# Kernel tuning notes

Hardware: AMD Instinct MI355X
Metric: run time of the kernel (lower is better)

## Reference

```python
import jax, jax.numpy as jnp
import numpy as np

N_E, N_U, N_D = 512, 256, 256
N_A = 16
N_FB = 4
N_SV = 256
N_PV = 64
D_IN0 = 3 * (4 * N_A) + 2 * 4   # 200, fb_block output at layer 0
D_IN = 3 * N_SV + 2 * N_PV      # 896, fb_block output thereafter


def _fb_block(s_v, p_v):
    # s_v: (n_e, d_s); p_v: (n_e, n_e, d_p)
    n_e = N_U + N_D
    su_m = jnp.tile(s_v[:N_U].mean(0)[None, :], (n_e, 1))
    sd_m = jnp.tile(s_v[N_U:].mean(0)[None, :], (n_e, 1))
    pu_m = p_v[:N_U].mean(0)   # (n_e, d_p)
    pd_m = p_v[N_U:].mean(0)
    return jnp.concatenate([su_m, sd_m, pu_m, pd_m, s_v], axis=-1)


def setup_inputs() -> dict:
    key = jax.random.key(0)
    ks = jax.random.split(key, 16)

    def lin(k, fin, fout):
        k1, k2 = jax.random.split(k)
        lim = 1.0 / np.sqrt(fin)
        W = jax.random.uniform(k1, (fin, fout), minval=-lim, maxval=lim, dtype=jnp.float32)
        b = jax.random.uniform(k2, (fout,), minval=-lim, maxval=lim, dtype=jnp.float32)
        return W, b

    V0_W, V0_b = lin(ks[0], D_IN0, N_SV)
    W0_W, W0_b = lin(ks[1], 4, N_PV)
    VrW, Vrb, WrW, Wrb = [], [], [], []
    for i in range(N_FB - 1):
        w, b = lin(ks[2 + i], D_IN, N_SV); VrW.append(w); Vrb.append(b)
        w, b = lin(ks[6 + i], N_PV, N_PV); WrW.append(w); Wrb.append(b)
    Vr_W, Vr_b = jnp.stack(VrW), jnp.stack(Vrb)
    Wr_W, Wr_b = jnp.stack(WrW), jnp.stack(Wrb)
    Vhu_W, Vhu_b = lin(ks[10], D_IN, N_SV)
    Vhd_W, Vhd_b = lin(ks[11], D_IN, N_SV)
    wu_W, wu_b = lin(ks[12], N_SV, N_U)
    wd_W, wd_b = lin(ks[13], N_SV, N_D)
    r = jax.random.normal(ks[14], (N_E, 3), dtype=jnp.float32)
    a = jax.random.normal(ks[15], (N_A, 3), dtype=jnp.float32) * 2.0
    return dict(r=r, a=a, V0_W=V0_W, V0_b=V0_b, Vr_W=Vr_W, Vr_b=Vr_b,
                W0_W=W0_W, W0_b=W0_b, Wr_W=Wr_W, Wr_b=Wr_b,
                Vhu_W=Vhu_W, Vhu_b=Vhu_b, Vhd_W=Vhd_W, Vhd_b=Vhd_b,
                wu_W=wu_W, wu_b=wu_b, wd_W=wd_W, wd_b=wd_b)


def reference(r, a, V0_W, V0_b, Vr_W, Vr_b, W0_W, W0_b, Wr_W, Wr_b,
              Vhu_W, Vhu_b, Vhd_W, Vhd_b, wu_W, wu_b, wd_W, wd_b):
    n_e = N_E
    eye = jnp.eye(n_e, dtype=r.dtype)[:, :, None]
    ra = r[:, None, :] - a[None, :, :]                       # (n_e, n_a, 3)
    ra_len = jnp.linalg.norm(ra, axis=-1, keepdims=True)
    rr = r[None, :, :] - r[:, None, :]                       # (n_e, n_e, 3)
    rr_len = jnp.linalg.norm(rr + eye, axis=-1, keepdims=True)
    s_v = jnp.concatenate([ra, ra_len], axis=-1).reshape(n_e, -1)   # (n_e, 4*n_a)
    p_v = jnp.concatenate([rr, rr_len], axis=-1)                    # (n_e, n_e, 4)
    s_blk = _fb_block(s_v, p_v)
    for l in range(N_FB):
        VW, Vb = (V0_W, V0_b) if l == 0 else (Vr_W[l - 1], Vr_b[l - 1])
        WW, Wb = (W0_W, W0_b) if l == 0 else (Wr_W[l - 1], Wr_b[l - 1])
        s_new = jnp.tanh(s_blk @ VW + Vb)
        s_v = s_new + s_v if s_v.shape[-1] == N_SV else s_new   # residual skips layer 0
        p_new = jnp.tanh(p_v @ WW + Wb)
        p_v = p_new + p_v if p_v.shape[-1] == N_PV else p_new
        s_blk = _fb_block(s_v, p_v)
    s_u = jnp.tanh(s_blk[:N_U] @ Vhu_W + Vhu_b)
    s_d = jnp.tanh(s_blk[N_U:] @ Vhd_W + Vhd_b)
    s_wu = s_u @ wu_W + wu_b                                  # (n_u, n_u)
    s_wd = s_d @ wd_W + wd_b                                  # (n_d, n_d)
    exp_u = jnp.linalg.norm(ra[:N_U], axis=-1, keepdims=True)  # (n_u, n_a, 1)
    exp_d = jnp.linalg.norm(ra[N_U:], axis=-1, keepdims=True)
    orb_u = (s_wu * jnp.exp(-exp_u).sum(axis=1))[None]         # (1, n_u, n_u)
    orb_d = (s_wd * jnp.exp(-exp_d).sum(axis=1))[None]
    # logabssumdet with n_det == 1, matrix dim > 1
    sgn_u, log_u = jnp.linalg.slogdet(orb_u)
    sgn_d, log_d = jnp.linalg.slogdet(orb_d)
    psi = (sgn_u * sgn_d * jnp.exp(log_u + log_d)).sum()
    return jnp.log(jnp.abs(psi))
```

## Files before the change

### kernel.cpp

```cpp
#include <hip/hip_runtime.h>
#include <hip/hip_bf16.h>

#define NE 512

__device__ __align__(16) float g_sv0[NE*64];
__device__ __align__(16) float g_sv[2][NE*256];
__device__ __align__(16) float g_pu4[NE*4];
__device__ __align__(16) float g_pd4[NE*4];
__device__ __align__(16) float g_puL[4*NE*64];
__device__ __align__(16) float g_pdL[4*NE*64];
__device__ __align__(16) float g_su0[64];
__device__ __align__(16) float g_sd0[64];
__device__ __align__(16) float g_part4[4*16*NE*64];
__device__ __align__(16) float g_spart[2][16*256];
__device__ __align__(16) float g_f[NE];
__device__ __align__(16) float g_hu[256*256];
__device__ __align__(16) float g_hd[256*256];
__device__ __align__(16) float g_orbu[256*256];
__device__ __align__(16) float g_orbd[256*256];
__device__ float g_logs[2];
__device__ unsigned g_ludone;

__device__ __forceinline__ float tanh_fast(float x) {
  float e = __expf(2.f * x);
  return 1.f - 2.f / (e + 1.f);
}

__global__ __launch_bounds__(256, 2) void k_front(const float* __restrict__ r,
                                                  const float* __restrict__ a,
                                                  const float* __restrict__ W0,
                                                  const float* __restrict__ b0,
                                                  const float* __restrict__ Wr,
                                                  const float* __restrict__ brs) {
  __shared__ __align__(16) float xrow[4*32*68];
  __shared__ __align__(16) float wtile[4096];
  __shared__ __align__(16) float msc[4*4*68];
  __shared__ float red[4][4];
  int bid = blockIdx.x, t = threadIdx.x;
  if (bid == 0 && t == 0) g_ludone = 0u;
  if (bid < 512) {
    int j = bid;
    if (j == 0) {
      for (int h = 0; h < 2; ++h) {
        int e = h*256 + t;
        float rx = r[3*e], ry = r[3*e+1], rz = r[3*e+2];
        float facc = 0.f;
        #pragma unroll
        for (int at = 0; at < 16; ++at) {
          float dx = rx - a[3*at], dy = ry - a[3*at+1], dz = rz - a[3*at+2];
          float len = sqrtf(dx*dx + dy*dy + dz*dz);
          g_sv0[e*64 + 4*at + 0] = dx;
          g_sv0[e*64 + 4*at + 1] = dy;
          g_sv0[e*64 + 4*at + 2] = dz;
          g_sv0[e*64 + 4*at + 3] = len;
          facc += expf(-len);
        }
        g_f[e] = facc;
      }
      __syncthreads();
      if (t < 128) {
        int h = t >> 6, c = t & 63;
        float s = 0.f;
        for (int i = 0; i < 256; ++i) s += g_sv0[(h*256 + i)*64 + c];
        (h ? g_sd0 : g_su0)[c] = s * (1.f/256.f);
      }
      __syncthreads();
    }
    float rjx = r[3*j], rjy = r[3*j+1], rjz = r[3*j+2];
    for (int h = 0; h < 2; ++h) {
      int i = h*256 + t;
      float dx = rjx - r[3*i], dy = rjy - r[3*i+1], dz = rjz - r[3*i+2];
      float ee = (i == j) ? 1.f : 0.f;
      float ex = dx+ee, ey = dy+ee, ez = dz+ee;
      float len = sqrtf(ex*ex + ey*ey + ez*ez);
      float v0 = dx, v1 = dy, v2 = dz, v3 = len;
      #pragma unroll
      for (int m = 1; m < 64; m <<= 1) {
        v0 += __shfl_xor(v0, m); v1 += __shfl_xor(v1, m);
        v2 += __shfl_xor(v2, m); v3 += __shfl_xor(v3, m);
      }
      if ((t & 63) == 0) {
        int wv = t >> 6;
        red[wv][0]=v0; red[wv][1]=v1; red[wv][2]=v2; red[wv][3]=v3;
      }
      __syncthreads();
      if (t == 0) {
        float* dst = h ? g_pd4 : g_pu4;
        #pragma unroll
        for (int c = 0; c < 4; ++c)
          dst[j*4 + c] = (red[0][c]+red[1][c]+red[2][c]+red[3][c]) * (1.f/256.f);
      }
      __syncthreads();
    }
  } else {
    int lane = t & 63, wv = t >> 6;
    int gw = (bid - 512)*4 + wv;
    int j = gw >> 4, chunk = gw & 15;
    int i0 = chunk * 32;
    int rg = lane >> 4, cg = lane & 15;
    float* xr = xrow + wv*(32*68);
    float* ms = msc + wv*(4*68);
    float rjx = r[3*j], rjy = r[3*j+1], rjz = r[3*j+2];
    float xres[8][4];
    {
      float4 w0 = *(const float4*)&W0[0*64 + 4*cg];
      float4 w1 = *(const float4*)&W0[1*64 + 4*cg];
      float4 w2 = *(const float4*)&W0[2*64 + 4*cg];
      float4 w3 = *(const float4*)&W0[3*64 + 4*cg];
      float4 bv = *(const float4*)&b0[4*cg];
      #pragma unroll
      for (int q = 0; q < 8; ++q) {
        int row = 4*q + rg;
        int i = i0 + row;
        float dx = rjx - r[3*i], dy = rjy - r[3*i+1], dz = rjz - r[3*i+2];
        float ee = (i == j) ? 1.f : 0.f;
        float ex = dx+ee, ey = dy+ee, ez = dz+ee;
        float len = sqrtf(ex*ex + ey*ey + ez*ez);
        float y0 = tanh_fast(bv.x + dx*w0.x + dy*w1.x + dz*w2.x + len*w3.x);
        float y1 = tanh_fast(bv.y + dx*w0.y + dy*w1.y + dz*w2.y + len*w3.y);
        float y2 = tanh_fast(bv.z + dx*w0.z + dy*w1.z + dz*w2.z + len*w3.z);
        float y3 = tanh_fast(bv.w + dx*w0.w + dy*w1.w + dz*w2.w + len*w3.w);
        xres[q][0]=y0; xres[q][1]=y1; xres[q][2]=y2; xres[q][3]=y3;
        float4 yv; yv.x=y0; yv.y=y1; yv.z=y2; yv.w=y3;
        *(float4*)&xr[row*68 + 4*cg] = yv;
      }
      float cs0=0,cs1=0,cs2=0,cs3=0;
      #pragma unroll
      for (int q=0;q<8;++q){cs0+=xres[q][0];cs1+=xres[q][1];cs2+=xres[q][2];cs3+=xres[q][3];}
      ms[rg*68+4*cg+0]=cs0; ms[rg*68+4*cg+1]=cs1;
      ms[rg*68+4*cg+2]=cs2; ms[rg*68+4*cg+3]=cs3;
      float tot = ms[0*68+lane]+ms[1*68+lane]+ms[2*68+lane]+ms[3*68+lane];
      g_part4[0*(16*NE*64) + chunk*(NE*64) + j*64 + lane] = tot;
    }
    for (int l = 0; l < 3; ++l) {
      __syncthreads();
      for (int idx = t; idx < 4096; idx += 256) wtile[idx] = Wr[l*4096 + idx];
      __syncthreads();
      float4 bv = *(const float4*)&brs[l*64 + 4*cg];
      float acc[8][4];
      #pragma unroll
      for (int q=0;q<8;++q){acc[q][0]=bv.x;acc[q][1]=bv.y;acc[q][2]=bv.z;acc[q][3]=bv.w;}
      #pragma unroll 4
      for (int kq = 0; kq < 16; ++kq) {
        float4 wv0 = *(const float4*)&wtile[(4*kq+0)*64 + 4*cg];
        float4 wv1 = *(const float4*)&wtile[(4*kq+1)*64 + 4*cg];
        float4 wv2 = *(const float4*)&wtile[(4*kq+2)*64 + 4*cg];
        float4 wv3 = *(const float4*)&wtile[(4*kq+3)*64 + 4*cg];
        #pragma unroll
        for (int q = 0; q < 8; ++q) {
          float4 xv = *(const float4*)&xr[(4*q+rg)*68 + 4*kq];
          acc[q][0] += xv.x*wv0.x + xv.y*wv1.x + xv.z*wv2.x + xv.w*wv3.x;
          acc[q][1] += xv.x*wv0.y + xv.y*wv1.y + xv.z*wv2.y + xv.w*wv3.y;
          acc[q][2] += xv.x*wv0.z + xv.y*wv1.z + xv.z*wv2.z + xv.w*wv3.z;
          acc[q][3] += xv.x*wv0.w + xv.y*wv1.w + xv.z*wv2.w + xv.w*wv3.w;
        }
      }
      float cs0=0,cs1=0,cs2=0,cs3=0;
      #pragma unroll
      for (int q = 0; q < 8; ++q) {
        float y0 = tanh_fast(acc[q][0]) + xres[q][0];
        float y1 = tanh_fast(acc[q][1]) + xres[q][1];
        float y2 = tanh_fast(acc[q][2]) + xres[q][2];
        float y3 = tanh_fast(acc[q][3]) + xres[q][3];
        xres[q][0]=y0; xres[q][1]=y1; xres[q][2]=y2; xres[q][3]=y3;
        float4 yv; yv.x=y0; yv.y=y1; yv.z=y2; yv.w=y3;
        *(float4*)&xr[(4*q+rg)*68 + 4*cg] = yv;
        cs0+=y0; cs1+=y1; cs2+=y2; cs3+=y3;
      }
      ms[rg*68+4*cg+0]=cs0; ms[rg*68+4*cg+1]=cs1;
      ms[rg*68+4*cg+2]=cs2; ms[rg*68+4*cg+3]=cs3;
      float tot = ms[0*68+lane]+ms[1*68+lane]+ms[2*68+lane]+ms[3*68+lane];
      g_part4[(l+1)*(16*NE*64) + chunk*(NE*64) + j*64 + lane] = tot;
    }
  }
}

__global__ __launch_bounds__(256) void k_reduce_p() {
  int idx = blockIdx.x*256 + threadIdx.x;
  int l = idx >> 16;
  int rem = idx & 65535;
  int half = rem >> 15;
  int r2 = rem & 32767;
  const float* pp = g_part4 + l*(16*NE*64) + half*(8*NE*64) + r2;
  float s = 0.f;
  #pragma unroll
  for (int ch = 0; ch < 8; ++ch) s += pp[ch*(NE*64)];
  (half ? g_pdL : g_puL)[l*(NE*64) + r2] = s * (1.f/256.f);
}

template<int PUK, int SVK, int MEANK>
__global__ __launch_bounds__(256) void k_smm(int which, const float* __restrict__ W,
                                             const float* __restrict__ Wb,
                                             const float* __restrict__ W2,
                                             const float* __restrict__ Wb2,
                                             int pl, int rsp, int wsp) {
  constexpr int MAINK = 2*PUK + SVK;
  __shared__ __align__(16) float wsl[MAINK*32];
  __shared__ float insl[32*(MAINK+1)];
  __shared__ float biasv[32];
  __shared__ float bred[256];
  __shared__ float susd[512];
  __shared__ float wred[4][8][4];
  const float *pu_p=nullptr, *pd_p=nullptr, *sv_p=nullptr, *su_p=nullptr, *sd_p=nullptr;
  const float *res_p=nullptr, *rs_p=nullptr;
  float* out_p = nullptr;
  int t = threadIdx.x;
  int rg = blockIdx.x, cg = blockIdx.y;
  int grp = 0, rgl = rg;
  if (which >= 4) { grp = rg >> 3; rgl = rg & 7; }
  const float* Wsel = (which >= 4 && grp) ? W2 : W;
  const float* Wbsel = (which >= 4 && grp) ? Wb2 : Wb;
  int in_base = 0, dotanh = 1;
  switch (which) {
    case 0: pu_p=g_pu4; pd_p=g_pd4; su_p=g_su0; sd_p=g_sd0; sv_p=g_sv0;
            out_p=g_sv[0]; in_base=rg*32; break;
    case 1: case 2: case 3:
      pu_p=g_puL + pl*(NE*64); pd_p=g_pdL + pl*(NE*64);
      sv_p=g_sv[(which+1)&1]; res_p=sv_p; out_p=g_sv[which&1]; in_base=rg*32; break;
    case 4: pu_p=g_puL + pl*(NE*64); pd_p=g_pdL + pl*(NE*64);
            sv_p=g_sv[1]; out_p = grp ? g_hd : g_hu; in_base = grp*256 + rgl*32; break;
    default: sv_p = grp ? g_hd : g_hu; out_p = grp ? g_orbd : g_orbu;
             rs_p = g_f + grp*256; in_base = rgl*32; dotanh = 0; break;
  }
  if (rsp >= 0 && MEANK == 256) {
    const float* sp = g_spart[rsp];
    for (int e = t; e < 512; e += 256) {
      int half = e >> 8, c = e & 255;
      float s = 0.f;
      #pragma unroll
      for (int g8 = 0; g8 < 8; ++g8) s += sp[(half*8 + g8)*256 + c];
      susd[e] = s * (1.f/256.f);
    }
    su_p = &susd[0]; sd_p = &susd[256];
    __syncthreads();
  }
  int out_base = (which >= 4) ? rgl*32 : rg*32;
  int col0 = cg * 32;
  for (int idx = t; idx < MAINK*32; idx += 256) {
    int c = idx >> 5, cl = idx & 31;
    wsl[idx] = Wsel[(2*MEANK + c)*256 + col0 + cl];
  }
  for (int rr = 0; rr < 32; ++rr) {
    int row = in_base + rr;
    for (int c = t; c < MAINK; c += 256) {
      float v;
      if (c < PUK) v = pu_p[row*PUK + c];
      else if (c < 2*PUK) v = pd_p[row*PUK + (c - PUK)];
      else v = sv_p[row*SVK + (c - 2*PUK)];
      insl[rr*(MAINK+1) + c] = v;
    }
  }
  {
    int pcol = t & 31, ps = t >> 5;
    float bacc = 0.f;
    if (MEANK > 0) {
      for (int c = ps; c < MEANK; c += 8)
        bacc += su_p[c]*Wsel[c*256 + col0 + pcol] + sd_p[c]*Wsel[(MEANK + c)*256 + col0 + pcol];
    }
    bred[ps*32 + pcol] = bacc;
  }
  __syncthreads();
  if (t < 32) {
    float s = Wbsel[col0 + t];
    #pragma unroll
    for (int p8 = 0; p8 < 8; ++p8) s += bred[p8*32 + t];
    biasv[t] = s;
  }
  __syncthreads();
  int c4 = t & 7, rl = t >> 3;
  float a0 = biasv[4*c4], a1 = biasv[4*c4+1], a2 = biasv[4*c4+2], a3 = biasv[4*c4+3];
  const float* inrow = &insl[rl*(MAINK+1)];
  #pragma unroll 4
  for (int c = 0; c < MAINK; ++c) {
    float iv = inrow[c];
    float4 wv = *(const float4*)&wsl[c*32 + 4*c4];
    a0 += iv*wv.x; a1 += iv*wv.y; a2 += iv*wv.z; a3 += iv*wv.w;
  }
  int rowA = out_base + rl;
  int col = col0 + 4*c4;
  if (dotanh) { a0=tanh_fast(a0); a1=tanh_fast(a1); a2=tanh_fast(a2); a3=tanh_fast(a3); }
  if (res_p) {
    float4 rv = *(const float4*)&res_p[rowA*256 + col];
    a0 += rv.x; a1 += rv.y; a2 += rv.z; a3 += rv.w;
  }
  if (rs_p) { float fsc = rs_p[rowA]; a0*=fsc; a1*=fsc; a2*=fsc; a3*=fsc; }
  float4 ov; ov.x=a0; ov.y=a1; ov.z=a2; ov.w=a3;
  *(float4*)&out_p[rowA*256 + col] = ov;
  if (wsp >= 0) {
    int lane = t & 63, wv = t >> 6;
    float s0=a0, s1=a1, s2=a2, s3=a3;
    #pragma unroll
    for (int m = 8; m < 64; m <<= 1) {
      s0 += __shfl_xor(s0, m); s1 += __shfl_xor(s1, m);
      s2 += __shfl_xor(s2, m); s3 += __shfl_xor(s3, m);
    }
    if ((lane >> 3) == 0) {
      wred[wv][c4][0]=s0; wred[wv][c4][1]=s1; wred[wv][c4][2]=s2; wred[wv][c4][3]=s3;
    }
    __syncthreads();
    if (t < 32) {
      int cc4 = t >> 2, cc = t & 3;
      float tot = wred[0][cc4][cc]+wred[1][cc4][cc]+wred[2][cc4][cc]+wred[3][cc4][cc];
      g_spart[wsp][rg*256 + col0 + 4*cc4 + cc] = tot;
    }
  }
}

#define REP8(M) M(0) M(1) M(2) M(3) M(4) M(5) M(6) M(7)
#define DPPMAX(v, CTRL) { unsigned _o = (unsigned)__builtin_amdgcn_update_dpp(0, (int)(v), CTRL, 0xf, 0xf, true); \
                          (v) = (v) > _o ? (v) : _o; }

__global__ __launch_bounds__(512, 2) void k_lu(float* __restrict__ out) {
  __shared__ __align__(16) float colbuf[2][256];
  __shared__ __align__(16) float prowbuf[2][16*20];
  const float* A = (blockIdx.x == 0) ? g_orbu : g_orbd;
  int t = threadIdx.x;
  int tile_c = t >> 5;
  int tile_r = t & 31;
  int lane = t & 63;
  int br = tile_r * 8;
  int pb = tile_c * 20;
  const float4* Ap = (const float4*)(A + br*256 + tile_c*16);
#define DECLROW(R) float4 M##R##_0 = Ap[R*64+0], M##R##_1 = Ap[R*64+1], \
                          M##R##_2 = Ap[R*64+2], M##R##_3 = Ap[R*64+3];
  REP8(DECLROW)
#undef DECLROW
  unsigned um = 0;
  if (tile_c == 0) {
#define INIT0(R) colbuf[0][br+R] = M##R##_0.x;
    REP8(INIT0)
#undef INIT0
  }
  __syncthreads();
  float prod = 1.f;
  int esum = 0;
  float m0=0,m1=0,m2=0,m3=0,m4=0,m5=0,m6=0,m7=0;
  for (int k = 0; k < 256; ++k) {
    const float* cbin = colbuf[k & 1];
    float4 cv = *(const float4*)&cbin[4*lane];
    float4 ca = *(const float4*)&cbin[br];
    float4 cb2 = *(const float4*)&cbin[br+4];
    bool aliveU = (tile_c*16 + 15) >= k;
    if (k > 0 && aliveU) {
      const float* pwp = &prowbuf[(k-1) & 1][pb];
      float4 P0 = *(const float4*)&pwp[0];
      float4 P1 = *(const float4*)&pwp[4];
      float4 P2 = *(const float4*)&pwp[8];
      float4 P3 = *(const float4*)&pwp[12];
#define UPD(R) { float mr = m##R; \
  M##R##_0.x -= mr*P0.x; M##R##_0.y -= mr*P0.y; M##R##_0.z -= mr*P0.z; M##R##_0.w -= mr*P0.w; \
  M##R##_1.x -= mr*P1.x; M##R##_1.y -= mr*P1.y; M##R##_1.z -= mr*P1.z; M##R##_1.w -= mr*P1.w; \
  M##R##_2.x -= mr*P2.x; M##R##_2.y -= mr*P2.y; M##R##_2.z -= mr*P2.z; M##R##_2.w -= mr*P2.w; \
  M##R##_3.x -= mr*P3.x; M##R##_3.y -= mr*P3.y; M##R##_3.z -= mr*P3.z; M##R##_3.w -= mr*P3.w; }
      REP8(UPD)
#undef UPD
    }
    unsigned b0 = (um & 1u) ? 0u : ((__float_as_uint(fabsf(cv.x)) & 0xFFFFFF00u) | (unsigned)(4*lane+0));
    unsigned b1 = (um & 2u) ? 0u : ((__float_as_uint(fabsf(cv.y)) & 0xFFFFFF00u) | (unsigned)(4*lane+1));
    unsigned b2 = (um & 4u) ? 0u : ((__float_as_uint(fabsf(cv.z)) & 0xFFFFFF00u) | (unsigned)(4*lane+2));
    unsigned b3 = (um & 8u) ? 0u : ((__float_as_uint(fabsf(cv.w)) & 0xFFFFFF00u) | (unsigned)(4*lane+3));
    unsigned bb = max(max(b0,b1), max(b2,b3));
    DPPMAX(bb, 0x111) DPPMAX(bb, 0x112) DPPMAX(bb, 0x114) DPPMAX(bb, 0x118)
    DPPMAX(bb, 0x142) DPPMAX(bb, 0x143)
    bb = (unsigned)__builtin_amdgcn_readlane((int)bb, 63);
    int p = (int)(bb & 255u);
    int wl = p >> 2, cc = p & 3;
    unsigned px = (unsigned)__builtin_amdgcn_readlane((int)__float_as_uint(cv.x), wl);
    unsigned py = (unsigned)__builtin_amdgcn_readlane((int)__float_as_uint(cv.y), wl);
    unsigned pz = (unsigned)__builtin_amdgcn_readlane((int)__float_as_uint(cv.z), wl);
    unsigned pw = (unsigned)__builtin_amdgcn_readlane((int)__float_as_uint(cv.w), wl);
    float piv = __uint_as_float(cc==0 ? px : cc==1 ? py : cc==2 ? pz : pw);
    int ee; float mant = frexpf(fabsf(piv), &ee);
    prod *= mant; esum += ee;
    int e2; prod = frexpf(prod, &e2); esum += e2;
    if (wl == lane) um |= 1u << cc;
    if (k == 255) break;
    float rp = 1.0f / piv;
    m0 = ca.x*rp; m1 = ca.y*rp; m2 = ca.z*rp; m3 = ca.w*rp;
    m4 = cb2.x*rp; m5 = cb2.y*rp; m6 = cb2.z*rp; m7 = cb2.w*rp;
    bool aliveK = (tile_c*16 + 15) > k;
    if (aliveK && tile_r == (p >> 3)) {
      float* pw_ = &prowbuf[k & 1][pb];
      switch (p & 7) {
#define PUBC(R) case R: *(float4*)&pw_[0] = M##R##_0; *(float4*)&pw_[4] = M##R##_1; \
                        *(float4*)&pw_[8] = M##R##_2; *(float4*)&pw_[12] = M##R##_3; break;
        REP8(PUBC)
#undef PUBC
      }
    }
    int kn = k + 1;
    if (tile_c == (kn >> 4)) {
      float e0,e1,e2b,e3,e4,e5,e6,e7;
      switch (kn & 15) {
#define EXTC(I, G, C) case I: e0=M0_##G.C; e1=M1_##G.C; e2b=M2_##G.C; e3=M3_##G.C; \
                              e4=M4_##G.C; e5=M5_##G.C; e6=M6_##G.C; e7=M7_##G.C; break;
        EXTC(0,0,x) EXTC(1,0,y) EXTC(2,0,z) EXTC(3,0,w)
        EXTC(4,1,x) EXTC(5,1,y) EXTC(6,1,z) EXTC(7,1,w)
        EXTC(8,2,x) EXTC(9,2,y) EXTC(10,2,z) EXTC(11,2,w)
        EXTC(12,3,x) EXTC(13,3,y) EXTC(14,3,z) EXTC(15,3,w)
#undef EXTC
      }
      float sel;
      switch (p & 7) {
        case 0: sel = e0; break; case 1: sel = e1; break;
        case 2: sel = e2b; break; case 3: sel = e3; break;
        case 4: sel = e4; break; case 5: sel = e5; break;
        case 6: sel = e6; break; default: sel = e7; break;
      }
      float pv = __shfl(sel, (tile_c & 1)*32 + (p >> 3), 64);
      float4 w0, w1;
      w0.x = e0 - m0*pv; w0.y = e1 - m1*pv; w0.z = e2b - m2*pv; w0.w = e3 - m3*pv;
      w1.x = e4 - m4*pv; w1.y = e5 - m5*pv; w1.z = e6 - m6*pv; w1.w = e7 - m7*pv;
      *(float4*)&colbuf[kn & 1][br] = w0;
      *(float4*)&colbuf[kn & 1][br+4] = w1;
    }
    __syncthreads();
  }
  if (t == 0) {
    float ls = logf(prod) + (float)esum * 0.69314718055994531f;
    __hip_atomic_store(&g_logs[blockIdx.x], ls, __ATOMIC_RELEASE, __HIP_MEMORY_SCOPE_AGENT);
    unsigned old = __hip_atomic_fetch_add(&g_ludone, 1u, __ATOMIC_ACQ_REL, __HIP_MEMORY_SCOPE_AGENT);
    if (old == 1u) {
      float l0 = __hip_atomic_load(&g_logs[0], __ATOMIC_ACQUIRE, __HIP_MEMORY_SCOPE_AGENT);
      float l1 = __hip_atomic_load(&g_logs[1], __ATOMIC_ACQUIRE, __HIP_MEMORY_SCOPE_AGENT);
      out[0] = l0 + l1;
    }
  }
}

extern "C" void kernel_launch(void* const* d_in, const int* in_sizes, int n_in,
                              void* d_out, int out_size, void* d_ws, size_t ws_size,
                              hipStream_t stream) {
  const float* r     = (const float*)d_in[0];
  const float* a     = (const float*)d_in[1];
  const float* V0_W  = (const float*)d_in[2];
  const float* V0_b  = (const float*)d_in[3];
  const float* Vr_W  = (const float*)d_in[4];
  const float* Vr_b  = (const float*)d_in[5];
  const float* W0_W  = (const float*)d_in[6];
  const float* W0_b  = (const float*)d_in[7];
  const float* Wr_W  = (const float*)d_in[8];
  const float* Wr_b  = (const float*)d_in[9];
  const float* Vhu_W = (const float*)d_in[10];
  const float* Vhu_b = (const float*)d_in[11];
  const float* Vhd_W = (const float*)d_in[12];
  const float* Vhd_b = (const float*)d_in[13];
  const float* wu_W  = (const float*)d_in[14];
  const float* wu_b  = (const float*)d_in[15];
  const float* wd_W  = (const float*)d_in[16];
  const float* wd_b  = (const float*)d_in[17];
  float* out = (float*)d_out;

  k_front<<<2560, 256, 0, stream>>>(r, a, W0_W, W0_b, Wr_W, Wr_b);
  k_reduce_p<<<1024, 256, 0, stream>>>();
  k_smm<4,64,64><<<dim3(16,8), 256, 0, stream>>>(0, V0_W, V0_b, nullptr, nullptr,
                                                 0, -1, 0);
  k_smm<64,256,256><<<dim3(16,8), 256, 0, stream>>>(1, Vr_W + 0*896*256, Vr_b + 0,
                                                    nullptr, nullptr, 0, 0, 1);
  k_smm<64,256,256><<<dim3(16,8), 256, 0, stream>>>(2, Vr_W + 1*896*256, Vr_b + 256,
                                                    nullptr, nullptr, 1, 1, 0);
  k_smm<64,256,256><<<dim3(16,8), 256, 0, stream>>>(3, Vr_W + 2*896*256, Vr_b + 512,
                                                    nullptr, nullptr, 2, 0, 1);
  k_smm<64,256,256><<<dim3(16,8), 256, 0, stream>>>(4, Vhu_W, Vhu_b, Vhd_W, Vhd_b,
                                                    3, 1, -1);
  k_smm<0,256,0><<<dim3(16,8), 256, 0, stream>>>(6, wu_W, wu_b, wd_W, wd_b,
                                                 0, -1, -1);
  k_lu<<<2, 512, 0, stream>>>(out);
}
```

Baseline: 610.1 us.

## Move LU pivot search into column producer and fold partial reduction into k_smm

```diff
diff --git a/kernel.cpp b/kernel.cpp
--- a/kernel.cpp
+++ b/kernel.cpp
@@ -175,19 +175,6 @@
   }
 }
 
-__global__ __launch_bounds__(256) void k_reduce_p() {
-  int idx = blockIdx.x*256 + threadIdx.x;
-  int l = idx >> 16;
-  int rem = idx & 65535;
-  int half = rem >> 15;
-  int r2 = rem & 32767;
-  const float* pp = g_part4 + l*(16*NE*64) + half*(8*NE*64) + r2;
-  float s = 0.f;
-  #pragma unroll
-  for (int ch = 0; ch < 8; ++ch) s += pp[ch*(NE*64)];
-  (half ? g_pdL : g_puL)[l*(NE*64) + r2] = s * (1.f/256.f);
-}
-
 template<int PUK, int SVK, int MEANK>
 __global__ __launch_bounds__(256) void k_smm(int which, const float* __restrict__ W,
                                              const float* __restrict__ Wb,
@@ -206,6 +193,22 @@
   float* out_p = nullptr;
   int t = threadIdx.x;
   int rg = blockIdx.x, cg = blockIdx.y;
+  if (which == 0) {
+    int fid = blockIdx.y*16 + blockIdx.x;
+    #pragma unroll
+    for (int rep = 0; rep < 8; ++rep) {
+      int idx = fid*2048 + rep*256 + t;
+      int l = idx >> 16;
+      int rem = idx & 65535;
+      int half = rem >> 15;
+      int r2 = rem & 32767;
+      const float* pp = g_part4 + l*(16*NE*64) + half*(8*NE*64) + r2;
+      float s = 0.f;
+      #pragma unroll
+      for (int ch = 0; ch < 8; ++ch) s += pp[ch*(NE*64)];
+      (half ? g_pdL : g_puL)[l*(NE*64) + r2] = s * (1.f/256.f);
+    }
+  }
   int grp = 0, rgl = rg;
   if (which >= 4) { grp = rg >> 3; rgl = rg & 7; }
   const float* Wsel = (which >= 4 && grp) ? W2 : W;
@@ -313,6 +316,8 @@
 __global__ __launch_bounds__(512, 2) void k_lu(float* __restrict__ out) {
   __shared__ __align__(16) float colbuf[2][256];
   __shared__ __align__(16) float prowbuf[2][16*20];
+  __shared__ unsigned scal_p[2];
+  __shared__ float scal_v[2];
   const float* A = (blockIdx.x == 0) ? g_orbu : g_orbd;
   int t = threadIdx.x;
   int tile_c = t >> 5;
@@ -325,24 +330,50 @@
                           M##R##_2 = Ap[R*64+2], M##R##_3 = Ap[R*64+3];
   REP8(DECLROW)
 #undef DECLROW
-  unsigned um = 0;
+  unsigned um8 = 0;
+#define CANDV(V, R) { unsigned kk = (um8 & (1u<<R)) ? 0u : ((__float_as_uint(fabsf(V)) & 0xFFFFFF00u) | (unsigned)(br + R)); \
+                      if (kk > key) key = kk; }
   if (tile_c == 0) {
-#define INIT0(R) colbuf[0][br+R] = M##R##_0.x;
-    REP8(INIT0)
-#undef INIT0
+    float e0 = M0_0.x, e1 = M1_0.x, e2 = M2_0.x, e3 = M3_0.x;
+    float e4 = M4_0.x, e5 = M5_0.x, e6 = M6_0.x, e7 = M7_0.x;
+    float4 w0; w0.x=e0; w0.y=e1; w0.z=e2; w0.w=e3;
+    float4 w1; w1.x=e4; w1.y=e5; w1.z=e6; w1.w=e7;
+    *(float4*)&colbuf[0][br] = w0;
+    *(float4*)&colbuf[0][br+4] = w1;
+    unsigned key = 0;
+    CANDV(e0,0) CANDV(e1,1) CANDV(e2,2) CANDV(e3,3)
+    CANDV(e4,4) CANDV(e5,5) CANDV(e6,6) CANDV(e7,7)
+    DPPMAX(key, 0x111) DPPMAX(key, 0x112) DPPMAX(key, 0x114) DPPMAX(key, 0x118)
+    DPPMAX(key, 0x142)
+    int srcl = __builtin_amdgcn_readfirstlane((lane & 32) | 31);
+    int p = (int)((unsigned)__builtin_amdgcn_readlane((int)key, srcl) & 255u);
+    if (tile_r == (p >> 3)) {
+      float val;
+      switch (p & 7) {
+        case 0: val=e0; break; case 1: val=e1; break; case 2: val=e2; break;
+        case 3: val=e3; break; case 4: val=e4; break; case 5: val=e5; break;
+        case 6: val=e6; break; default: val=e7; break;
+      }
+      scal_v[0] = val;
+    }
+    if ((lane & 31) == 0) scal_p[0] = (unsigned)p;
   }
   __syncthreads();
   float prod = 1.f;
   int esum = 0;
   float m0=0,m1=0,m2=0,m3=0,m4=0,m5=0,m6=0,m7=0;
   for (int k = 0; k < 256; ++k) {
-    const float* cbin = colbuf[k & 1];
-    float4 cv = *(const float4*)&cbin[4*lane];
-    float4 ca = *(const float4*)&cbin[br];
-    float4 cb2 = *(const float4*)&cbin[br+4];
+    int buf = k & 1;
+    unsigned pk = scal_p[buf];
+    float piv = scal_v[buf];
+    int ee; float mant = frexpf(fabsf(piv), &ee);
+    prod *= mant; esum += ee;
+    int e2n; prod = frexpf(prod, &e2n); esum += e2n;
+    if ((int)(pk >> 3) == tile_r) um8 |= 1u << (pk & 7);
+    if (k == 255) break;
     bool aliveU = (tile_c*16 + 15) >= k;
     if (k > 0 && aliveU) {
-      const float* pwp = &prowbuf[(k-1) & 1][pb];
+      const float* pwp = &prowbuf[buf^1][pb];
       float4 P0 = *(const float4*)&pwp[0];
       float4 P1 = *(const float4*)&pwp[4];
       float4 P2 = *(const float4*)&pwp[8];
@@ -355,32 +386,15 @@
       REP8(UPD)
 #undef UPD
     }
-    unsigned b0 = (um & 1u) ? 0u : ((__float_as_uint(fabsf(cv.x)) & 0xFFFFFF00u) | (unsigned)(4*lane+0));
-    unsigned b1 = (um & 2u) ? 0u : ((__float_as_uint(fabsf(cv.y)) & 0xFFFFFF00u) | (unsigned)(4*lane+1));
-    unsigned b2 = (um & 4u) ? 0u : ((__float_as_uint(fabsf(cv.z)) & 0xFFFFFF00u) | (unsigned)(4*lane+2));
-    unsigned b3 = (um & 8u) ? 0u : ((__float_as_uint(fabsf(cv.w)) & 0xFFFFFF00u) | (unsigned)(4*lane+3));
-    unsigned bb = max(max(b0,b1), max(b2,b3));
-    DPPMAX(bb, 0x111) DPPMAX(bb, 0x112) DPPMAX(bb, 0x114) DPPMAX(bb, 0x118)
-    DPPMAX(bb, 0x142) DPPMAX(bb, 0x143)
-    bb = (unsigned)__builtin_amdgcn_readlane((int)bb, 63);
-    int p = (int)(bb & 255u);
-    int wl = p >> 2, cc = p & 3;
-    unsigned px = (unsigned)__builtin_amdgcn_readlane((int)__float_as_uint(cv.x), wl);
-    unsigned py = (unsigned)__builtin_amdgcn_readlane((int)__float_as_uint(cv.y), wl);
-    unsigned pz = (unsigned)__builtin_amdgcn_readlane((int)__float_as_uint(cv.z), wl);
-    unsigned pw = (unsigned)__builtin_amdgcn_readlane((int)__float_as_uint(cv.w), wl);
-    float piv = __uint_as_float(cc==0 ? px : cc==1 ? py : cc==2 ? pz : pw);
-    int ee; float mant = frexpf(fabsf(piv), &ee);
-    prod *= mant; esum += ee;
-    int e2; prod = frexpf(prod, &e2); esum += e2;
-    if (wl == lane) um |= 1u << cc;
-    if (k == 255) break;
     float rp = 1.0f / piv;
+    float4 ca = *(const float4*)&colbuf[buf][br];
+    float4 cb2 = *(const float4*)&colbuf[buf][br+4];
     m0 = ca.x*rp; m1 = ca.y*rp; m2 = ca.z*rp; m3 = ca.w*rp;
     m4 = cb2.x*rp; m5 = cb2.y*rp; m6 = cb2.z*rp; m7 = cb2.w*rp;
+    int p = (int)pk;
     bool aliveK = (tile_c*16 + 15) > k;
     if (aliveK && tile_r == (p >> 3)) {
-      float* pw_ = &prowbuf[k & 1][pb];
+      float* pw_ = &prowbuf[buf][pb];
       switch (p & 7) {
 #define PUBC(R) case R: *(float4*)&pw_[0] = M##R##_0; *(float4*)&pw_[4] = M##R##_1; \
                         *(float4*)&pw_[8] = M##R##_2; *(float4*)&pw_[12] = M##R##_3; break;
@@ -408,14 +422,33 @@
         case 6: sel = e6; break; default: sel = e7; break;
       }
       float pv = __shfl(sel, (tile_c & 1)*32 + (p >> 3), 64);
-      float4 w0, w1;
-      w0.x = e0 - m0*pv; w0.y = e1 - m1*pv; w0.z = e2b - m2*pv; w0.w = e3 - m3*pv;
-      w1.x = e4 - m4*pv; w1.y = e5 - m5*pv; w1.z = e6 - m6*pv; w1.w = e7 - m7*pv;
-      *(float4*)&colbuf[kn & 1][br] = w0;
-      *(float4*)&colbuf[kn & 1][br+4] = w1;
+      float w0x = e0 - m0*pv, w0y = e1 - m1*pv, w0z = e2b - m2*pv, w0w = e3 - m3*pv;
+      float w1x = e4 - m4*pv, w1y = e5 - m5*pv, w1z = e6 - m6*pv, w1w = e7 - m7*pv;
+      float4 w0; w0.x=w0x; w0.y=w0y; w0.z=w0z; w0.w=w0w;
+      float4 w1; w1.x=w1x; w1.y=w1y; w1.z=w1z; w1.w=w1w;
+      *(float4*)&colbuf[buf^1][br]   = w0;
+      *(float4*)&colbuf[buf^1][br+4] = w1;
+      unsigned key = 0;
+      CANDV(w0x,0) CANDV(w0y,1) CANDV(w0z,2) CANDV(w0w,3)
+      CANDV(w1x,4) CANDV(w1y,5) CANDV(w1z,6) CANDV(w1w,7)
+      DPPMAX(key, 0x111) DPPMAX(key, 0x112) DPPMAX(key, 0x114) DPPMAX(key, 0x118)
+      DPPMAX(key, 0x142)
+      int srcl = __builtin_amdgcn_readfirstlane((lane & 32) | 31);
+      int pn = (int)((unsigned)__builtin_amdgcn_readlane((int)key, srcl) & 255u);
+      if (tile_r == (pn >> 3)) {
+        float val;
+        switch (pn & 7) {
+          case 0: val=w0x; break; case 1: val=w0y; break; case 2: val=w0z; break;
+          case 3: val=w0w; break; case 4: val=w1x; break; case 5: val=w1y; break;
+          case 6: val=w1z; break; default: val=w1w; break;
+        }
+        scal_v[buf^1] = val;
+      }
+      if ((lane & 31) == 0) scal_p[buf^1] = (unsigned)pn;
     }
     __syncthreads();
   }
+#undef CANDV
   if (t == 0) {
     float ls = logf(prod) + (float)esum * 0.69314718055994531f;
     __hip_atomic_store(&g_logs[blockIdx.x], ls, __ATOMIC_RELEASE, __HIP_MEMORY_SCOPE_AGENT);
@@ -452,7 +485,6 @@
   float* out = (float*)d_out;
 
   k_front<<<2560, 256, 0, stream>>>(r, a, W0_W, W0_b, Wr_W, Wr_b);
-  k_reduce_p<<<1024, 256, 0, stream>>>();
   k_smm<4,64,64><<<dim3(16,8), 256, 0, stream>>>(0, V0_W, V0_b, nullptr, nullptr,
                                                  0, -1, 0);
   k_smm<64,256,256><<<dim3(16,8), 256, 0, stream>>>(1, Vr_W + 0*896*256, Vr_b + 0,
```

New measurement: 665.0 us. 9.0% more time.
